# Kernel optimization log

Measured on AMD Instinct MI355X. Metric: run time of the kernel, lower is better.

## Reference

```python
import jax, jax.numpy as jnp
import numpy as np

NEG_SLOPE = 0.2
NUM_HEADS = 8
HEAD_DIM = 16


def setup_inputs() -> dict:
    key = jax.random.key(0)
    ks = jax.random.split(key, 14)
    n_nodes, n_edges = 50000, 800000
    in_f, out_f, e_f, H, D = 256, 128, 64, NUM_HEADS, HEAD_DIM
    s = lambda fan_in: 1.0 / np.sqrt(fan_in)
    return {
        "node_features": jax.random.normal(ks[0], (n_nodes, in_f), jnp.float32),
        "edge_index": jax.random.randint(ks[1], (2, n_edges), 0, n_nodes),
        "edge_features": jax.random.normal(ks[2], (n_edges, e_f), jnp.float32),
        "Wl": jax.random.normal(ks[3], (in_f, out_f), jnp.float32) * s(in_f),
        "bl": jnp.zeros((out_f,), jnp.float32),
        "Wr": jax.random.normal(ks[4], (in_f, out_f), jnp.float32) * s(in_f),
        "br": jnp.zeros((out_f,), jnp.float32),
        "We": jax.random.normal(ks[5], (e_f, H), jnp.float32) * s(e_f),
        "be": jnp.zeros((H,), jnp.float32),
        "attn_vector": jax.random.normal(ks[6], (H, D), jnp.float32) * 0.01,
        "Wv": jax.random.normal(ks[7], (in_f, out_f), jnp.float32) * s(in_f),
        "bv": jnp.zeros((out_f,), jnp.float32),
        "Wo": jax.random.normal(ks[8], (out_f, out_f), jnp.float32) * s(out_f),
        "bo": jnp.zeros((out_f,), jnp.float32),
    }


def reference(node_features, edge_index, edge_features,
              Wl, bl, Wr, br, We, be, attn_vector, Wv, bv, Wo, bo):
    n_nodes = node_features.shape[0]
    n_edges = edge_index.shape[1]
    H, D = attn_vector.shape
    sources, targets = edge_index[0], edge_index[1]

    # node projections: [N, H, D]
    left = (node_features @ Wl + bl).reshape(n_nodes, H, D)
    right = (node_features @ Wr + br).reshape(n_nodes, H, D)

    # per-edge GATv2 score: a^T LeakyReLU(W_l h_t + W_r h_s) + edge bias
    combined = left[targets] + right[sources]                      # [E, H, D]
    activated = jax.nn.leaky_relu(combined, negative_slope=NEG_SLOPE)
    attn_scores = jnp.einsum("ehd,hd->eh", activated, attn_vector)  # [E, H]
    attn_scores = attn_scores + (edge_features @ We + be)

    # segment softmax over incoming edges per target node
    max_scores = jax.ops.segment_max(attn_scores, targets, num_segments=n_nodes)
    attn_exp = jnp.exp(attn_scores - max_scores[targets])
    attn_sum = jax.ops.segment_sum(attn_exp, targets, num_segments=n_nodes) + 1e-10
    attn_probs = attn_exp / attn_sum[targets]                      # [E, H]

    # weighted scatter-aggregate of values
    values = (node_features @ Wv + bv).reshape(n_nodes, H, D)
    weighted = attn_probs[:, :, None] * values[sources]            # [E, H, D]
    aggregated = jax.ops.segment_sum(
        weighted.reshape(n_edges, H * D), targets, num_segments=n_nodes)
    return aggregated @ Wo + bo
```

## Files before the change

### kernel.cpp

```cpp
#include <hip/hip_runtime.h>
#include <hip/hip_bf16.h>
#include <stdint.h>

#define NUM_H 8
#define DIM 16
#define HD 128
#define IN_F 256
#define E_F 64
#define NEG_SLOPE 0.2f
#define NB 8
#define EB 32

#define NCT 24
#define KSTEPS 8
#define WELEMS (KSTEPS * NCT * 64 * 8)

typedef __bf16 bf16x8 __attribute__((ext_vector_type(8)));
typedef float f32x4 __attribute__((ext_vector_type(4)));
typedef short short8 __attribute__((ext_vector_type(8)));

__device__ __forceinline__ float b2f(__hip_bfloat16 x) { return __bfloat162float(x); }
__device__ __forceinline__ __hip_bfloat16 f2b(float x) { return __float2bfloat16(x); }
__device__ __forceinline__ float bs2f(short s) {
    uint32_t u = ((uint32_t)(uint16_t)s) << 16;
    return __builtin_bit_cast(float, u);
}

__global__ void k_zero_int(int* p, int n) {
    int i = blockIdx.x * blockDim.x + threadIdx.x;
    int stride = gridDim.x * blockDim.x;
    for (; i < n; i += stride) p[i] = 0;
}

__global__ void k_hist(const int* __restrict__ eidx, int* __restrict__ deg, int n_edges) {
    int e = blockIdx.x * blockDim.x + threadIdx.x;
    if (e < n_edges) atomicAdd(&deg[eidx[n_edges + e]], 1);
}

__global__ void k_scan(const int* __restrict__ deg, int* __restrict__ offs,
                       int* __restrict__ cursor, int n) {
    __shared__ int part[1024];
    int tid = threadIdx.x;
    int chunk = (n + 1023) / 1024;
    int base = tid * chunk;
    int hi = base + chunk < n ? base + chunk : n;
    int sum = 0;
    for (int i = base; i < hi; i++) sum += deg[i];
    part[tid] = sum;
    __syncthreads();
    for (int off = 1; off < 1024; off <<= 1) {
        int v = (tid >= off) ? part[tid - off] : 0;
        __syncthreads();
        part[tid] += v;
        __syncthreads();
    }
    int run = (tid == 0) ? 0 : part[tid - 1];
    for (int i = base; i < hi; i++) {
        offs[i] = run;
        cursor[i] = run;
        run += deg[i];
    }
    if (tid == 0) offs[n] = part[1023];
}

__global__ void k_wprep(const float* __restrict__ Wl, const float* __restrict__ Wr,
                        const float* __restrict__ Wv,
                        __bf16* __restrict__ Whi, __bf16* __restrict__ Wlo) {
    int tid = blockIdx.x * blockDim.x + threadIdx.x;
    if (tid >= KSTEPS * NCT * 64) return;
    int l = tid & 63;
    int ctks = tid >> 6;
    int ct = ctks % NCT;
    int ks = ctks / NCT;
    int gc = ct * 16 + (l & 15);
    int m = gc >> 7;
    int c = gc & 127;
    const float* W = (m == 0) ? Wl : (m == 1) ? Wr : Wv;
    bf16x8 h8, l8;
#pragma unroll
    for (int i = 0; i < 8; i++) {
        int k = ks * 32 + ((l >> 4) << 3) + i;
        float w = W[k * HD + c];
        __bf16 hi = (__bf16)w;
        __bf16 lo = (__bf16)(w - (float)hi);
        h8[i] = hi;
        l8[i] = lo;
    }
    *(bf16x8*)(Whi + (size_t)tid * 8) = h8;
    *(bf16x8*)(Wlo + (size_t)tid * 8) = l8;
}

__global__ __launch_bounds__(256, 2) void k_projm(
    const float* __restrict__ nf,
    const __bf16* __restrict__ Whi, const __bf16* __restrict__ Wlo,
    const float* __restrict__ bl, const float* __restrict__ br,
    const float* __restrict__ bv,
    __hip_bfloat16* __restrict__ left, __hip_bfloat16* __restrict__ right,
    __hip_bfloat16* __restrict__ val, int n_nodes) {
    int l = threadIdx.x & 63;
    int wave = threadIdx.x >> 6;
    int row0 = blockIdx.x * 64 + wave * 16;
    if (row0 >= n_nodes) return;
    int lr = l & 15, lg = l >> 4;
    const float* arow = nf + (size_t)(row0 + lr) * IN_F + lg * 8;

    const f32x4 zero = {0.f, 0.f, 0.f, 0.f};
    f32x4 acc[NCT];
#pragma unroll
    for (int ct = 0; ct < NCT; ct++) acc[ct] = zero;

    for (int ks = 0; ks < KSTEPS; ks++) {
        f32x4 a0 = *(const f32x4*)(arow + ks * 32);
        f32x4 a1 = *(const f32x4*)(arow + ks * 32 + 4);
        bf16x8 ah, al;
#pragma unroll
        for (int i = 0; i < 4; i++) {
            __bf16 h = (__bf16)a0[i];
            ah[i] = h;
            al[i] = (__bf16)(a0[i] - (float)h);
        }
#pragma unroll
        for (int i = 0; i < 4; i++) {
            __bf16 h = (__bf16)a1[i];
            ah[4 + i] = h;
            al[4 + i] = (__bf16)(a1[i] - (float)h);
        }
        const bf16x8* wh = (const bf16x8*)(Whi) + (size_t)ks * NCT * 64 + l;
        const bf16x8* wl = (const bf16x8*)(Wlo) + (size_t)ks * NCT * 64 + l;
#pragma unroll
        for (int ct = 0; ct < NCT; ct++) {
            bf16x8 bh = wh[ct * 64];
            bf16x8 blo = wl[ct * 64];
            acc[ct] = __builtin_amdgcn_mfma_f32_16x16x32_bf16(ah, bh, acc[ct], 0, 0, 0);
            acc[ct] = __builtin_amdgcn_mfma_f32_16x16x32_bf16(al, bh, acc[ct], 0, 0, 0);
            acc[ct] = __builtin_amdgcn_mfma_f32_16x16x32_bf16(ah, blo, acc[ct], 0, 0, 0);
        }
    }

#pragma unroll
    for (int ct = 0; ct < NCT; ct++) {
        const int m = ct >> 3;
        int c = ((ct & 7) << 4) + lr;
        float bias = (m == 0) ? bl[c] : (m == 1) ? br[c] : bv[c];
        __hip_bfloat16* dst = (m == 0) ? left : (m == 1) ? right : val;
#pragma unroll
        for (int r = 0; r < 4; r++) {
            int row = row0 + lg * 4 + r;
            dst[(size_t)row * HD + c] = f2b(acc[ct][r] + bias);
        }
    }
}

__global__ __launch_bounds__(256) void k_escore(
    const int* __restrict__ eidx, const float* __restrict__ ef,
    const float* __restrict__ We, const float* __restrict__ be,
    const float* __restrict__ av,
    const __hip_bfloat16* __restrict__ left,
    const __hip_bfloat16* __restrict__ right,
    int* __restrict__ cursor, int* __restrict__ srcs,
    __hip_bfloat16* __restrict__ es_csr, int n_edges) {
    __shared__ float sef[EB][68];
    int tid = threadIdx.x;
    int e0 = blockIdx.x * EB;
    {
        const f32x4* src = (const f32x4*)(ef + (size_t)e0 * E_F);
        int lim = (n_edges - e0) * (E_F / 4);
        if (lim > EB * (E_F / 4)) lim = EB * (E_F / 4);
#pragma unroll 2
        for (int i = tid; i < lim; i += 256) {
            f32x4 v = src[i];
            int le = i >> 4;
            int k = (i & 15) << 2;
            *(f32x4*)&sef[le][k] = v;
        }
    }
    __syncthreads();
    int le = tid >> 3;
    int h = tid & 7;
    int e = e0 + le;
    if (e >= n_edges) return;
    int s = eidx[e];
    int t = eidx[n_edges + e];

    int lane = tid & 63;
    int pos = 0;
    if (h == 0) pos = atomicAdd(&cursor[t], 1);
    pos = __shfl(pos, lane & ~7);

    float sc = be[h];
    const float* row = &sef[le][0];
#pragma unroll
    for (int k4 = 0; k4 < E_F / 4; k4++) {
        f32x4 v = *(const f32x4*)(row + k4 * 4);
        sc += v[0] * We[(k4 * 4 + 0) * NUM_H + h] + v[1] * We[(k4 * 4 + 1) * NUM_H + h] +
              v[2] * We[(k4 * 4 + 2) * NUM_H + h] + v[3] * We[(k4 * 4 + 3) * NUM_H + h];
    }

    const short8* Lp = (const short8*)(left + (size_t)t * HD + h * DIM);
    const short8* Rp = (const short8*)(right + (size_t)s * HD + h * DIM);
    short8 l0 = Lp[0], l1 = Lp[1];
    short8 r0 = Rp[0], r1 = Rp[1];
    const float* avh = av + h * DIM;
#pragma unroll
    for (int d = 0; d < 8; d++) {
        float x = bs2f(l0[d]) + bs2f(r0[d]);
        x = x > 0.0f ? x : NEG_SLOPE * x;
        sc += x * avh[d];
    }
#pragma unroll
    for (int d = 0; d < 8; d++) {
        float x = bs2f(l1[d]) + bs2f(r1[d]);
        x = x > 0.0f ? x : NEG_SLOPE * x;
        sc += x * avh[8 + d];
    }
    if (h == 0) srcs[pos] = s;
    es_csr[(size_t)pos * NUM_H + h] = f2b(expf(sc));
}

__global__ __launch_bounds__(64) void k_agg(
    const int* __restrict__ offs, const int* __restrict__ srcs,
    const __hip_bfloat16* __restrict__ es_csr,
    const __hip_bfloat16* __restrict__ val,
    float* __restrict__ nagg, int n_nodes) {
    int t = blockIdx.x;
    if (t >= n_nodes) return;
    int lane = threadIdx.x;
    int sub = lane >> 4;
    int c16 = lane & 15;
    int h = c16 >> 1;
    int beg = offs[t], end = offs[t + 1];

    float acc[8] = {0.f, 0.f, 0.f, 0.f, 0.f, 0.f, 0.f, 0.f};
    float wsum = 0.0f;
#pragma unroll 2
    for (int i0 = beg; i0 < end; i0 += 4) {
        int i = i0 + sub;
        bool act = i < end;
        int ii = act ? i : beg;
        int s = srcs[ii];
        float w = b2f(es_csr[(size_t)ii * NUM_H + h]);
        if (!act) w = 0.0f;
        short8 v = *(const short8*)(val + (size_t)s * HD + c16 * 8);
        wsum += w;
#pragma unroll
        for (int d = 0; d < 8; d++) acc[d] += w * bs2f(v[d]);
    }
#pragma unroll
    for (int m = 16; m <= 32; m <<= 1) {
        wsum += __shfl_xor(wsum, m);
#pragma unroll
        for (int d = 0; d < 8; d++) acc[d] += __shfl_xor(acc[d], m);
    }
    if (sub == 0) {
        float inv = 1.0f / (wsum + 1e-10f);
        f32x4 o0, o1;
#pragma unroll
        for (int d = 0; d < 4; d++) { o0[d] = acc[d] * inv; o1[d] = acc[4 + d] * inv; }
        float* dst = nagg + (size_t)t * HD + c16 * 8;
        *(f32x4*)dst = o0;
        *(f32x4*)(dst + 4) = o1;
    }
}

__global__ void k_out(const float* __restrict__ nagg, const float* __restrict__ Wo,
                      const float* __restrict__ bo, float* __restrict__ out, int n_nodes) {
    __shared__ float srow[NB][HD];
    int node0 = blockIdx.x * NB;
    int j = threadIdx.x;
    for (int i = j; i < NB * HD; i += 128)
        srow[i / HD][i % HD] = nagg[(size_t)node0 * HD + i];
    __syncthreads();
    float a[NB];
    float b = bo[j];
#pragma unroll
    for (int n = 0; n < NB; n++) a[n] = b;
    for (int k = 0; k < HD; k++) {
        float w = Wo[k * HD + j];
#pragma unroll
        for (int n = 0; n < NB; n++) a[n] += srow[n][k] * w;
    }
#pragma unroll
    for (int n = 0; n < NB; n++) out[(size_t)(node0 + n) * HD + j] = a[n];
}

extern "C" void kernel_launch(void* const* d_in, const int* in_sizes, int n_in,
                              void* d_out, int out_size, void* d_ws, size_t ws_size,
                              hipStream_t stream) {
    const float* nf = (const float*)d_in[0];
    const int* eidx = (const int*)d_in[1];
    const float* ef = (const float*)d_in[2];
    const float* Wl = (const float*)d_in[3];
    const float* bl = (const float*)d_in[4];
    const float* Wr = (const float*)d_in[5];
    const float* br = (const float*)d_in[6];
    const float* We = (const float*)d_in[7];
    const float* be = (const float*)d_in[8];
    const float* av = (const float*)d_in[9];
    const float* Wv = (const float*)d_in[10];
    const float* bv = (const float*)d_in[11];
    const float* Wo = (const float*)d_in[12];
    const float* bo = (const float*)d_in[13];
    float* out = (float*)d_out;

    const int n_nodes = in_sizes[0] / IN_F;
    const int n_edges = in_sizes[1] / 2;
    const size_t NHD = (size_t)n_nodes * HD;

    char* base = (char*)d_ws;
    __hip_bfloat16* left  = (__hip_bfloat16*)(base + 256);
    __hip_bfloat16* right = left + NHD;
    __hip_bfloat16* es_csr = right + NHD;
    int* deg    = (int*)(es_csr + (size_t)n_edges * NUM_H);
    int* offs   = deg + n_nodes;
    int* cursor = offs + n_nodes + 1;
    int* srcs   = cursor + n_nodes;
    __bf16* Whi = (__bf16*)es_csr;
    __bf16* Wlo = Whi + (size_t)WELEMS;
    float* nagg = (float*)left;
    __hip_bfloat16* val = (__hip_bfloat16*)d_out;

    int eb = (n_edges + 255) / 256;

    k_wprep<<<(KSTEPS * NCT * 64 + 255) / 256, 256, 0, stream>>>(Wl, Wr, Wv, Whi, Wlo);

    k_zero_int<<<64, 256, 0, stream>>>(deg, n_nodes);
    k_hist<<<eb, 256, 0, stream>>>(eidx, deg, n_edges);
    k_scan<<<1, 1024, 0, stream>>>(deg, offs, cursor, n_nodes);

    k_projm<<<(n_nodes + 63) / 64, 256, 0, stream>>>(nf, Whi, Wlo, bl, br, bv,
                                                     left, right, val, n_nodes);

    k_escore<<<(n_edges + EB - 1) / EB, 256, 0, stream>>>(
        eidx, ef, We, be, av, left, right, cursor, srcs, es_csr, n_edges);

    k_agg<<<n_nodes, 64, 0, stream>>>(offs, srcs, es_csr, val, nagg, n_nodes);

    k_out<<<n_nodes / NB, 128, 0, stream>>>(nagg, Wo, bo, out, n_nodes);
}
```

Measured before the change: 779.9 us.

## Split edge-score kernel into edge-feature dot and gather/permute passes

The fused edge-score kernel is split in two. The first kernel computes the edge-feature projection and stores a bf16 partial score per edge and head. The second kernel does the left/right gather, LeakyReLU and attention dot, then scatters into CSR order through the atomic cursor. This separates the streaming edge-feature read from the random gathers, so each kernel can reach higher occupancy. The cost is an extra launch and an extra write and read of the partial scores. es_csr moves into the output buffer region, which adds a bf16 rounding of the partial score.

```diff
diff --git a/kernel.cpp b/kernel.cpp
--- a/kernel.cpp
+++ b/kernel.cpp
@@ -151,14 +151,9 @@
     }
 }
 
-__global__ __launch_bounds__(256) void k_escore(
-    const int* __restrict__ eidx, const float* __restrict__ ef,
-    const float* __restrict__ We, const float* __restrict__ be,
-    const float* __restrict__ av,
-    const __hip_bfloat16* __restrict__ left,
-    const __hip_bfloat16* __restrict__ right,
-    int* __restrict__ cursor, int* __restrict__ srcs,
-    __hip_bfloat16* __restrict__ es_csr, int n_edges) {
+__global__ __launch_bounds__(256) void k_edot(
+    const float* __restrict__ ef, const float* __restrict__ We,
+    const float* __restrict__ be, __hip_bfloat16* __restrict__ sp, int n_edges) {
     __shared__ float sef[EB][68];
     int tid = threadIdx.x;
     int e0 = blockIdx.x * EB;
@@ -169,9 +164,7 @@
 #pragma unroll 2
         for (int i = tid; i < lim; i += 256) {
             f32x4 v = src[i];
-            int le = i >> 4;
-            int k = (i & 15) << 2;
-            *(f32x4*)&sef[le][k] = v;
+            *(f32x4*)&sef[i >> 4][(i & 15) << 2] = v;
         }
     }
     __syncthreads();
@@ -179,14 +172,6 @@
     int h = tid & 7;
     int e = e0 + le;
     if (e >= n_edges) return;
-    int s = eidx[e];
-    int t = eidx[n_edges + e];
-
-    int lane = tid & 63;
-    int pos = 0;
-    if (h == 0) pos = atomicAdd(&cursor[t], 1);
-    pos = __shfl(pos, lane & ~7);
-
     float sc = be[h];
     const float* row = &sef[le][0];
 #pragma unroll
@@ -195,7 +180,29 @@
         sc += v[0] * We[(k4 * 4 + 0) * NUM_H + h] + v[1] * We[(k4 * 4 + 1) * NUM_H + h] +
               v[2] * We[(k4 * 4 + 2) * NUM_H + h] + v[3] * We[(k4 * 4 + 3) * NUM_H + h];
     }
-
+    sp[(size_t)e * NUM_H + h] = f2b(sc);
+}
+
+__global__ __launch_bounds__(256) void k_gperm(
+    const int* __restrict__ eidx, const __hip_bfloat16* __restrict__ sp,
+    const __hip_bfloat16* __restrict__ left,
+    const __hip_bfloat16* __restrict__ right,
+    const float* __restrict__ av,
+    int* __restrict__ cursor, int* __restrict__ srcs,
+    __hip_bfloat16* __restrict__ es_csr, int n_edges) {
+    int gid = blockIdx.x * blockDim.x + threadIdx.x;
+    int e = gid >> 3;
+    int h = gid & 7;
+    if (e >= n_edges) return;
+    int s = eidx[e];
+    int t = eidx[n_edges + e];
+
+    int lane = threadIdx.x & 63;
+    int pos = 0;
+    if (h == 0) pos = atomicAdd(&cursor[t], 1);
+    pos = __shfl(pos, lane & ~7);
+
+    float sc = b2f(sp[(size_t)e * NUM_H + h]);
     const short8* Lp = (const short8*)(left + (size_t)t * HD + h * DIM);
     const short8* Rp = (const short8*)(right + (size_t)s * HD + h * DIM);
     short8 l0 = Lp[0], l1 = Lp[1];
@@ -309,15 +316,16 @@
     char* base = (char*)d_ws;
     __hip_bfloat16* left  = (__hip_bfloat16*)(base + 256);
     __hip_bfloat16* right = left + NHD;
-    __hip_bfloat16* es_csr = right + NHD;
-    int* deg    = (int*)(es_csr + (size_t)n_edges * NUM_H);
+    __hip_bfloat16* sp    = right + NHD;
+    int* deg    = (int*)(sp + (size_t)n_edges * NUM_H);
     int* offs   = deg + n_nodes;
     int* cursor = offs + n_nodes + 1;
     int* srcs   = cursor + n_nodes;
-    __bf16* Whi = (__bf16*)es_csr;
+    __bf16* Whi = (__bf16*)sp;
     __bf16* Wlo = Whi + (size_t)WELEMS;
     float* nagg = (float*)left;
     __hip_bfloat16* val = (__hip_bfloat16*)d_out;
+    __hip_bfloat16* es_csr = val + NHD;
 
     int eb = (n_edges + 255) / 256;
 
@@ -330,8 +338,10 @@
     k_projm<<<(n_nodes + 63) / 64, 256, 0, stream>>>(nf, Whi, Wlo, bl, br, bv,
                                                      left, right, val, n_nodes);
 
-    k_escore<<<(n_edges + EB - 1) / EB, 256, 0, stream>>>(
-        eidx, ef, We, be, av, left, right, cursor, srcs, es_csr, n_edges);
+    k_edot<<<(n_edges + EB - 1) / EB, 256, 0, stream>>>(ef, We, be, sp, n_edges);
+
+    k_gperm<<<((size_t)n_edges * NUM_H + 255) / 256, 256, 0, stream>>>(
+        eidx, sp, left, right, av, cursor, srcs, es_csr, n_edges);
 
     k_agg<<<n_nodes, 64, 0, stream>>>(offs, srcs, es_csr, val, nagg, n_nodes);
 
```

New measurement: 744.3 us. -4.6%, faster.
